# Optimization experiments

Measured on AMD Instinct MI355X. Metric: run time of the kernel, lower is better.

Reference implementation:

```python
import jax, jax.numpy as jnp
import numpy as np

N_NODES = 50000
N_GRAPHS = 500
BLOCK = N_NODES // N_GRAPHS  # 100 nodes per graph
N_EDGES = 800000
D = 32        # emb_dim = in_feat = out_feat
H = 4         # num_heads
R = 16        # num relations
N_CODES = 20000
L = 2         # n_layers
SLOPE = 0.2
LAM = 0.5     # loop_lambda


def setup_inputs() -> dict:
    key = jax.random.key(0)
    ks = jax.random.split(key, 20)
    node_ids = jax.random.randint(ks[0], (N_NODES,), 0, N_CODES)
    src = jax.random.randint(ks[1], (N_EDGES,), 0, N_NODES)
    # dst must live in the same graph as src (contiguous blocks of BLOCK nodes)
    off = jax.random.randint(ks[2], (N_EDGES,), 0, BLOCK)
    dst = (src // BLOCK) * BLOCK + off
    rel_type = jax.random.randint(ks[3], (N_EDGES,), 0, R)
    node2graph = jnp.repeat(jnp.arange(N_GRAPHS), BLOCK)
    state = jax.random.normal(ks[4], (N_GRAPHS, D), dtype=jnp.float32)
    readout_weight = jax.random.uniform(ks[5], (N_NODES,), dtype=jnp.float32)
    s = 1.0 / np.sqrt(D)
    code_emb = jax.random.uniform(ks[6], (N_CODES, D), minval=-1.0, maxval=1.0)
    rel_table = jax.random.uniform(ks[7], (R, D), minval=-1.0, maxval=1.0)
    W = jax.random.normal(ks[8], (L, R, D, D)) * s       # per-relation weights
    h_bias = jnp.zeros((L, D))
    Wr = jax.random.normal(ks[9], (L, D, H * D)) * s     # fc_rel_att
    br = jnp.zeros((L, H * D))
    We = jax.random.normal(ks[10], (L, D, H * D)) * s    # fc_edge_att
    be = jnp.zeros((L, H * D))
    attn_h = jax.random.normal(ks[11], (L, H, D)) * s
    attn_t = jax.random.normal(ks[12], (L, H, D)) * s
    attn_s = jax.random.normal(ks[13], (L, H, D)) * s
    attn_r = jax.random.normal(ks[14], (L, H, D)) * s
    attn_rs = jax.random.normal(ks[15], (L, H, D)) * s
    return dict(state=state, readout_weight=readout_weight, code_emb=code_emb,
                rel_table=rel_table, W=W, h_bias=h_bias, Wr=Wr, br=br, We=We, be=be,
                attn_h=attn_h, attn_t=attn_t, attn_s=attn_s, attn_r=attn_r, attn_rs=attn_rs,
                node_ids=node_ids, src=src, dst=dst, rel_type=rel_type, node2graph=node2graph)


def _forward(state, readout_weight, code_emb, rel_table, W, h_bias, Wr, br, We, be,
             attn_h, attn_t, attn_s, attn_r, attn_rs, node_ids, src, dst, rel_type, node2graph):
    lrelu = lambda x: jax.nn.leaky_relu(x, SLOPE)
    h = code_emb[node_ids]                      # [N, D]
    N = h.shape[0]
    G = state.shape[0]
    g_src = node2graph[src]                     # [E]
    rel_att = edge_att = None
    for l in range(L):
        # ---- relation attention (cal_rel_att, state path) ----
        rp = (rel_table @ Wr[l] + br[l]).reshape(R, H, D)
        sp = (state @ Wr[l] + br[l]).reshape(G, H, D)
        er = (rp * attn_r[l]).sum(-1)                       # [R, H]
        es = (sp * attn_rs[l]).sum(-1)                      # [G, H]
        ra = jax.nn.softmax(lrelu(er[None, :, :] + es[:, None, :]), axis=1)  # [G, R, H]
        rel_att = ra[g_src, rel_type]                       # [E, H]
        # ---- edge attention (cal_edge_att, state path) ----
        hp = (h @ We[l] + be[l]).reshape(N, H, D)           # multi-head src feat
        eh = (hp * attn_h[l]).sum(-1)                       # [N, H]
        et = (hp * attn_t[l]).sum(-1)                       # [N, H]
        nsp = (state[node2graph] @ We[l] + be[l]).reshape(N, H, D)
        esn = (nsp * attn_s[l]).sum(-1)                     # [N, H]
        e = lrelu(esn[src] + eh[src] + et[dst])             # [E, H]
        emax = jax.ops.segment_max(e, dst, num_segments=N)
        ex = jnp.exp(e - emax[dst])
        den = jax.ops.segment_sum(ex, dst, num_segments=N)
        edge_att = ex / den[dst]                            # edge_softmax over dst
        # ---- per-relation message: matmul(h_src, W[etype]) ----
        # transform all nodes per relation, then gather (same math as per-edge bmm)
        hW = jnp.einsum('nhd,rde->rnhe', hp, W[l])          # [R, N, H, D]
        msg = hW[rel_type, src]                             # [E, H, D]
        msg = (msg * edge_att[..., None] * rel_att[..., None]).sum(axis=1)  # [E, D]
        agg = jax.ops.segment_sum(msg, dst, num_segments=N) + h_bias[l]
        h = jax.nn.relu((1.0 - LAM) * agg + LAM * h)        # self-loop blend + relu
    x = jax.ops.segment_sum(h * readout_weight[:, None], node2graph, num_segments=G)
    return x, rel_att, edge_att


def reference(state, readout_weight, code_emb, rel_table, W, h_bias, Wr, br, We, be,
              attn_h, attn_t, attn_s, attn_r, attn_rs, node_ids, src, dst, rel_type, node2graph):
    return _forward(state, readout_weight, code_emb, rel_table, W, h_bias, Wr, br, We, be,
                    attn_h, attn_t, attn_s, attn_r, attn_rs, node_ids, src, dst, rel_type, node2graph)
```

## Files before the change

kernel.cpp:

```cpp
#include <hip/hip_runtime.h>
#include <hip/hip_fp16.h>

#define DI __device__ __forceinline__

constexpr int NGRAPH = 500;
constexpr int EDGES  = 800000;
constexpr int NNODE  = 50000;
constexpr int CAP    = 56;

constexpr size_t WI_CURS  = 0;
constexpr size_t WI_SMETA = 50048;
constexpr size_t WF_PREP  = WI_SMETA + (size_t)NNODE * CAP;
constexpr size_t WF_WFRAG = WF_PREP + 672;

constexpr int S_H    = 0;
constexpr int S_HP   = 8000;
constexpr int S_U    = 33600;
constexpr int S_EH   = 136800;
constexpr int S_ET   = 138400;
constexpr int S_DEN  = 140000;
constexpr int S_RA   = 141600;
constexpr int S_ESG  = 141856;
constexpr int S_AH   = 141872;
constexpr int S_AT   = 142384;
constexpr int S_MLDS = 142896;
constexpr int S_RP   = 151088;
constexpr int S_TOTAL = 151496;
constexpr int UROW = 516;

typedef _Float16 f16x8 __attribute__((ext_vector_type(8)));
typedef float f32x4 __attribute__((ext_vector_type(4)));

DI float lrelu(float x) { return x >= 0.f ? x : 0.2f * x; }
DI f16x8 u4_to_f16x8(uint4 u) { f16x8 r; __builtin_memcpy(&r, &u, 16); return r; }
DI f16x8 two_u2(uint2 a, uint2 b) { return u4_to_f16x8(make_uint4(a.x, a.y, b.x, b.y)); }
DI float h2f(unsigned short u) { __half hv; __builtin_memcpy(&hv, &u, 2); return __half2float(hv); }

DI int hpIdx(int n, int c) { return n * 128 + (c ^ ((n & 7) << 3)); }

__global__ void k_scatter(const int* __restrict__ src, const int* __restrict__ dst,
                          const int* __restrict__ rt, int* __restrict__ curs,
                          int* __restrict__ smeta) {
    int e = blockIdx.x * 256 + threadIdx.x;
    if (e >= EDGES) return;
    int s = src[e], d = dst[e], r = rt[e];
    int g = (unsigned)d / 100u;
    int pos = atomicAdd(&curs[d], 1);
    if (pos < CAP)
        smeta[(size_t)d * CAP + pos] = (s - g * 100) | (r << 7) | (e << 11);
}

__global__ void k_setup(const float* __restrict__ rel_table, const float* __restrict__ Wr,
                        const float* __restrict__ br, const float* __restrict__ We,
                        const float* __restrict__ be, const float* __restrict__ attn_r,
                        const float* __restrict__ attn_rs, const float* __restrict__ attn_s,
                        const float* __restrict__ W, float* __restrict__ prep,
                        uint4* __restrict__ wf) {
    __shared__ float wra[2][32][4];
    __shared__ float sbias[2][3][4];
    int b = blockIdx.x, t = threadIdx.x;
    if (b == 0) {
        {
            int l = t >> 7, k = (t >> 2) & 31, h = t & 3;
            float a = 0.f, bb = 0.f, c = 0.f;
            for (int d2 = 0; d2 < 32; ++d2) {
                float w1 = Wr[(size_t)(l*32 + k)*128 + h*32 + d2];
                float w2 = We[(size_t)(l*32 + k)*128 + h*32 + d2];
                a  += w1 * attn_r [l*128 + h*32 + d2];
                bb += w1 * attn_rs[l*128 + h*32 + d2];
                c  += w2 * attn_s [l*128 + h*32 + d2];
            }
            wra[l][k][h] = a;
            prep[128 + (l*32 + k)*4 + h] = bb;
            prep[384 + (l*32 + k)*4 + h] = c;
        }
        if (t < 24) {
            int l = t / 12, which = (t % 12) / 4, h = t % 4;
            const float* bp = (which == 2) ? be : br;
            const float* ap = (which == 0) ? attn_r : (which == 1 ? attn_rs : attn_s);
            float s = 0.f;
            for (int d2 = 0; d2 < 32; ++d2) s += bp[l*128 + h*32 + d2] * ap[l*128 + h*32 + d2];
            sbias[l][which][h] = s;
        }
        __syncthreads();
        if (t < 128) {
            int l = t >> 6, r = (t >> 2) & 15, h = t & 3;
            float s = sbias[l][0][h];
            for (int k = 0; k < 32; ++k) s += rel_table[r*32 + k] * wra[l][k][h];
            prep[(l*16 + r)*4 + h] = s;
        }
        if (t < 8) {
            int l = t >> 2, h = t & 3;
            prep[640 + l*4 + h] = sbias[l][1][h];
            prep[648 + l*4 + h] = sbias[l][2][h];
        }
    } else if (b <= 16) {
        int fi = (b - 1) * 256 + t;
        int ln = fi & 63, Nt = (fi >> 6) & 1, rel = (fi >> 7) & 15, l = fi >> 11;
        int j = Nt*16 + (ln & 15), k0 = (ln >> 4) << 3;
        unsigned short fr[8];
        #pragma unroll
        for (int i = 0; i < 8; ++i) {
            __half hv = __float2half(W[(((size_t)l*16 + rel)*32 + k0 + i)*32 + j]);
            __builtin_memcpy(&fr[i], &hv, 2);
        }
        uint4 o;
        o.x = fr[0] | ((unsigned)fr[1] << 16);
        o.y = fr[2] | ((unsigned)fr[3] << 16);
        o.z = fr[4] | ((unsigned)fr[5] << 16);
        o.w = fr[6] | ((unsigned)fr[7] << 16);
        wf[fi] = o;
    } else {
        int fi = (b - 17) * 256 + t;
        int ln = fi & 63, Nt = (fi >> 6) & 7, l = fi >> 9;
        int c = Nt*16 + (ln & 15);
        int phys = (c & 3)*32 + (c >> 2);
        int k0 = (ln >> 4) << 3;
        unsigned short fr[8];
        #pragma unroll
        for (int i = 0; i < 8; ++i) {
            __half hv = __float2half(We[(size_t)l*4096 + (k0 + i)*128 + phys]);
            __builtin_memcpy(&fr[i], &hv, 2);
        }
        uint4 o;
        o.x = fr[0] | ((unsigned)fr[1] << 16);
        o.y = fr[2] | ((unsigned)fr[3] << 16);
        o.z = fr[4] | ((unsigned)fr[5] << 16);
        o.w = fr[6] | ((unsigned)fr[7] << 16);
        wf[4096 + fi] = o;
    }
}

__global__ void __launch_bounds__(1024, 1)
k_fused(const float* __restrict__ state, const float* __restrict__ rw,
        const float* __restrict__ code_emb, const float* __restrict__ h_bias,
        const float* __restrict__ be, const float* __restrict__ attn_h,
        const float* __restrict__ attn_t, const int* __restrict__ node_ids,
        const int* __restrict__ curs, const int* __restrict__ smeta,
        const float* __restrict__ prep, const uint4* __restrict__ wf,
        float* __restrict__ xout, float* __restrict__ relOut, float* __restrict__ edgeOut) {
    extern __shared__ char smem[];
    __half* hH  = (__half*)(smem + S_H);
    __half* hpH = (__half*)(smem + S_HP);
    __half* Uh  = (__half*)(smem + S_U);
    float* ehp  = (float*)(smem + S_EH);
    float* etp  = (float*)(smem + S_ET);
    float* denp = (float*)(smem + S_DEN);
    float* rap  = (float*)(smem + S_RA);
    float* esgp = (float*)(smem + S_ESG);
    float* sAH  = (float*)(smem + S_AH);
    float* sAT  = (float*)(smem + S_AT);
    int*   mlds = (int*)(smem + S_MLDS);
    int*   rp   = (int*)(smem + S_RP);
    const uint4* wfe = wf + 4096;

    const int g = blockIdx.x;
    const int t = threadIdx.x;
    const int lane = t & 63, w = t >> 6;
    const int ln15 = lane & 15, q = lane >> 4, q8 = q << 3;
    const int MtA = w % 7, NtA = w / 7;
    const bool hasT = (w < 14);
    const int cg = w >> 1;
    const int colc = cg * 16 + ln15;
    const int physc = (colc & 3) * 32 + (colc >> 2);
    const int Mt0 = (w & 1) ? 4 : 0;
    const int Mt1 = (w & 1) ? 7 : 4;

    for (int i = t; i < 1600; i += 1024) {
        int n = i >> 4, dp = i & 15;
        int id = node_ids[g * 100 + n];
        float2 v = *(const float2*)&code_emb[(size_t)id * 32 + dp * 2];
        *(__half2*)&hH[n * 40 + dp * 2] = __floats2half2_rn(v.x, v.y);
    }
    if (t < 100) { int c = curs[g * 100 + t]; rp[t + 1] = c < CAP ? c : CAP; }
    if (t == 0) rp[0] = 0;
    __syncthreads();
    for (int o = 1; o < 128; o <<= 1) {
        int v = 0;
        if (t <= 100 && t >= o) v = rp[t - o];
        __syncthreads();
        if (t <= 100 && t >= o) rp[t] += v;
        __syncthreads();
    }
    for (int i = t; i < 100 * CAP; i += 1024) {
        int bin = i / CAP, pos = i % CAP;
        int lo = rp[bin], cnt = rp[bin + 1] - lo;
        if (pos < cnt)
            mlds[lo + pos] = smeta[(size_t)(g * 100 + bin) * CAP + pos];
    }

    for (int l = 0; l < 2; ++l) {
        __syncthreads();

        for (int i = t; i < 6450; i += 1024) ((uint4*)(smem + S_U))[i] = make_uint4(0, 0, 0, 0);
        if (t < 128) {
            sAH[t] = attn_h[l * 128 + (t & 3) * 32 + (t >> 2)];
            sAT[t] = attn_t[l * 128 + (t & 3) * 32 + (t >> 2)];
        }
        {
            uint4 bwe = wfe[(l * 8 + cg) * 64 + lane];
            f16x8 bw = u4_to_f16x8(bwe);
            float beC = be[l * 128 + physc];
            f32x4 z = {0.f, 0.f, 0.f, 0.f};
            for (int Mt = Mt0; Mt < Mt1; ++Mt) {
                const __half* hr = hH + (Mt * 16 + ln15) * 40 + q8;
                f32x4 pc = __builtin_amdgcn_mfma_f32_16x16x32_f16(
                    two_u2(*(const uint2*)hr, *(const uint2*)(hr + 4)), bw, z, 0, 0, 0);
                #pragma unroll
                for (int i = 0; i < 4; ++i) {
                    int n = Mt * 16 + q * 4 + i;
                    if (n < 100) hpH[hpIdx(n, colc)] = __float2half(pc[i] + beC);
                }
            }
        }
        {
            int k32 = lane & 31;
            float sG = state[g * 32 + k32];
            float4 frs = *(const float4*)&prep[128 + l * 128 + k32 * 4];
            float4 fes = *(const float4*)&prep[384 + l * 128 + k32 * 4];
            float p0 = sG * frs.x, p1 = sG * frs.y, p2 = sG * frs.z, p3 = sG * frs.w;
            float q0 = sG * fes.x, q1 = sG * fes.y, q2 = sG * fes.z, q3 = sG * fes.w;
            #pragma unroll
            for (int m = 1; m < 32; m <<= 1) {
                p0 += __shfl_xor(p0, m); p1 += __shfl_xor(p1, m);
                p2 += __shfl_xor(p2, m); p3 += __shfl_xor(p3, m);
                q0 += __shfl_xor(q0, m); q1 += __shfl_xor(q1, m);
                q2 += __shfl_xor(q2, m); q3 += __shfl_xor(q3, m);
            }
            int h = lane & 3;
            float esh  = (h & 2) ? ((h & 1) ? p3 : p2) : ((h & 1) ? p1 : p0);
            float esgh = (h & 2) ? ((h & 1) ? q3 : q2) : ((h & 1) ? q1 : q0);
            esh  += prep[640 + l * 4 + h];
            esgh += prep[648 + l * 4 + h];
            if (lane < 4) esgp[lane] = esgh;
            float er = prep[l * 64 + lane];
            float ex = __expf(lrelu(er + esh));
            float s = ex;
            s += __shfl_xor(s, 4); s += __shfl_xor(s, 8);
            s += __shfl_xor(s, 16); s += __shfl_xor(s, 32);
            rap[lane] = ex / s;
        }
        __syncthreads();

        if (t < 100) {
            int s = t;
            int sw = (s & 7) << 3;
            float eh[4] = {0, 0, 0, 0}, et[4] = {0, 0, 0, 0};
            #pragma unroll 4
            for (int i = 0; i < 16; ++i) {
                uint4 hv = *(const uint4*)&hpH[s * 128 + ((i * 8) ^ sw)];
                unsigned short hu[8];
                __builtin_memcpy(hu, &hv, 16);
                #pragma unroll
                for (int k = 0; k < 8; ++k) {
                    float f = h2f(hu[k]);
                    eh[k & 3] += f * sAH[i * 8 + k];
                    et[k & 3] += f * sAT[i * 8 + k];
                }
            }
            *(float4*)&ehp[s * 4] = make_float4(eh[0], eh[1], eh[2], eh[3]);
            *(float4*)&etp[s * 4] = make_float4(et[0], et[1], et[2], et[3]);
        }
        __syncthreads();

        if (t < 400) {
            int d = t >> 2, h = t & 3;
            int lo = rp[d], hi = rp[d + 1];
            float etd = etp[d * 4 + h] + esgp[h];
            float den = 0.f;
            for (int e = lo; e < hi; ++e) {
                int m = mlds[e];
                den += __expf(lrelu(ehp[(m & 127) * 4 + h] + etd));
            }
            denp[d * 4 + h] = den;
            if (l == 1) {
                float inv = 1.f / den;
                for (int e = lo; e < hi; ++e) {
                    int m = mlds[e];
                    float x = __expf(lrelu(ehp[(m & 127) * 4 + h] + etd));
                    int oe = (m >> 11) & 0xFFFFF;
                    int r = (m >> 7) & 15;
                    edgeOut[(size_t)oe * 4 + h] = x * inv;
                    relOut[(size_t)oe * 4 + h] = rap[r * 4 + h];
                }
            }
        }
        __syncthreads();

        if (t < 800) {
            int d = t >> 3, j = t & 7;
            int lo = rp[d], hi = rp[d + 1];
            float4 et4 = *(const float4*)&etp[d * 4];
            float4 esg4 = *(const float4*)esgp;
            float e0 = et4.x + esg4.x, e1 = et4.y + esg4.y;
            float e2 = et4.z + esg4.z, e3 = et4.w + esg4.w;
            float4 dn = *(const float4*)&denp[d * 4];
            float i0 = 1.f / dn.x, i1 = 1.f / dn.y, i2 = 1.f / dn.z, i3 = 1.f / dn.w;
            for (int e = lo; e < hi; ++e) {
                int m = mlds[e];
                int s = m & 127, r = (m >> 7) & 15;
                float4 eh4 = *(const float4*)&ehp[s * 4];
                float4 r4 = *(const float4*)&rap[r * 4];
                float c0 = __expf(lrelu(eh4.x + e0)) * i0 * r4.x;
                float c1 = __expf(lrelu(eh4.y + e1)) * i1 * r4.y;
                float c2 = __expf(lrelu(eh4.z + e2)) * i2 * r4.z;
                float c3 = __expf(lrelu(eh4.w + e3)) * i3 * r4.w;
                int sw = (s & 7) << 3;
                uint4 hv0 = *(const uint4*)&hpH[s * 128 + ((j * 16) ^ sw)];
                uint4 hv1 = *(const uint4*)&hpH[s * 128 + ((j * 16 + 8) ^ sw)];
                unsigned short hu[16];
                __builtin_memcpy(hu, &hv0, 16);
                __builtin_memcpy(hu + 8, &hv1, 16);
                float v0 = c0*h2f(hu[0])  + c1*h2f(hu[1])  + c2*h2f(hu[2])  + c3*h2f(hu[3]);
                float v1 = c0*h2f(hu[4])  + c1*h2f(hu[5])  + c2*h2f(hu[6])  + c3*h2f(hu[7]);
                float v2 = c0*h2f(hu[8])  + c1*h2f(hu[9])  + c2*h2f(hu[10]) + c3*h2f(hu[11]);
                float v3 = c0*h2f(hu[12]) + c1*h2f(hu[13]) + c2*h2f(hu[14]) + c3*h2f(hu[15]);
                __half* up = Uh + d * UROW + r * 32 + j * 4;
                __half2 u01 = *(__half2*)up;
                __half2 u23 = *(__half2*)(up + 2);
                float2 f01 = __half22float2(u01), f23 = __half22float2(u23);
                *(__half2*)up       = __floats2half2_rn(f01.x + v0, f01.y + v1);
                *(__half2*)(up + 2) = __floats2half2_rn(f23.x + v2, f23.y + v3);
            }
        }
        __syncthreads();

        f32x4 accA = {0.f, 0.f, 0.f, 0.f};
        if (hasT) {
            #pragma unroll 4
            for (int rel = 0; rel < 16; ++rel) {
                uint4 bAu = wf[((l * 16 + rel) * 2 + NtA) * 64 + lane];
                const __half* up = Uh + (MtA * 16 + ln15) * UROW + rel * 32 + q8;
                f16x8 af = two_u2(*(const uint2*)up, *(const uint2*)(up + 4));
                accA = __builtin_amdgcn_mfma_f32_16x16x32_f16(af, u4_to_f16x8(bAu), accA, 0, 0, 0);
            }
        }
        if (hasT) {
            int dcol = NtA * 16 + ln15;
            float bias = h_bias[l * 32 + dcol];
            #pragma unroll
            for (int i = 0; i < 4; ++i) {
                int n = MtA * 16 + q * 4 + i;
                if (n < 100) {
                    float hold = __half2float(hH[n * 40 + dcol]);
                    float hn = fmaxf(0.f, 0.5f * (accA[i] + bias) + 0.5f * hold);
                    hH[n * 40 + dcol] = __float2half(hn);
                }
            }
        }
    }
    __syncthreads();

    float* redp = (float*)(smem + S_U);
    {
        int part = t >> 5, d = t & 31;
        float acc = 0.f;
        for (int n = part; n < 100; n += 32)
            acc += __half2float(hH[n * 40 + d]) * rw[g * 100 + n];
        redp[part * 32 + d] = acc;
    }
    __syncthreads();
    if (t < 32) {
        float s = 0.f;
        #pragma unroll
        for (int p = 0; p < 32; ++p) s += redp[p * 32 + t];
        xout[g * 32 + t] = s;
    }
}

extern "C" void kernel_launch(void* const* d_in, const int* in_sizes, int n_in,
                              void* d_out, int out_size, void* d_ws, size_t ws_size,
                              hipStream_t stream) {
    const float* state     = (const float*)d_in[0];
    const float* rw        = (const float*)d_in[1];
    const float* code_emb  = (const float*)d_in[2];
    const float* rel_table = (const float*)d_in[3];
    const float* W         = (const float*)d_in[4];
    const float* h_bias    = (const float*)d_in[5];
    const float* Wr        = (const float*)d_in[6];
    const float* br        = (const float*)d_in[7];
    const float* We        = (const float*)d_in[8];
    const float* be        = (const float*)d_in[9];
    const float* attn_h    = (const float*)d_in[10];
    const float* attn_t    = (const float*)d_in[11];
    const float* attn_s    = (const float*)d_in[12];
    const float* attn_r    = (const float*)d_in[13];
    const float* attn_rs   = (const float*)d_in[14];
    const int* node_ids    = (const int*)d_in[15];
    const int* src         = (const int*)d_in[16];
    const int* dst         = (const int*)d_in[17];
    const int* rtype       = (const int*)d_in[18];

    float* out = (float*)d_out;
    float* xout = out;
    float* relOut = out + (size_t)NGRAPH * 32;
    float* edgeOut = relOut + (size_t)EDGES * 4;

    int* wsi = (int*)d_ws;
    float* wsf = (float*)d_ws;
    int* curs   = wsi + WI_CURS;
    int* smeta  = wsi + WI_SMETA;
    float* prep = wsf + WF_PREP;
    uint4* wfrag = (uint4*)(wsf + WF_WFRAG);

    (void)hipMemsetAsync(curs, 0, NNODE * sizeof(int), stream);
    k_scatter<<<(EDGES + 255) / 256, 256, 0, stream>>>(src, dst, rtype, curs, smeta);
    k_setup<<<21, 256, 0, stream>>>(rel_table, Wr, br, We, be, attn_r, attn_rs, attn_s,
                                    W, prep, wfrag);

    (void)hipFuncSetAttribute((const void*)k_fused, hipFuncAttributeMaxDynamicSharedMemorySize, S_TOTAL);
    k_fused<<<NGRAPH, 1024, S_TOTAL, stream>>>(state, rw, code_emb, h_bias, be,
                                               attn_h, attn_t, node_ids, curs, smeta,
                                               prep, wfrag, xout, relOut, edgeOut);
}
```

Measured before the change: 195.8 us.

## Merge scatter and setup kernels, fuse attention output writes, use fdot2 aggregation

Merges the edge-scatter and weight-setup kernels into a single launch, using block index ranges to pick the role. The layer-1 edge_att and rel_att output writes move out of the denominator loop and into the message loop, done by one lane per destination as float4 stores, so the exponentials are no longer computed twice. The per-edge message accumulation now packs the four head coefficients to fp16 and uses fdot2 with half2 adds instead of per-element half-to-float conversions. Rounding the coefficients to fp16 before the dot product adds some precision loss.

```diff
diff --git a/kernel.cpp b/kernel.cpp
--- a/kernel.cpp
+++ b/kernel.cpp
@@ -7,6 +7,7 @@
 constexpr int EDGES  = 800000;
 constexpr int NNODE  = 50000;
 constexpr int CAP    = 56;
+constexpr int SCAT_BLOCKS = (EDGES + 255) / 256;
 
 constexpr size_t WI_CURS  = 0;
 constexpr size_t WI_SMETA = 50048;
@@ -29,6 +30,7 @@
 constexpr int UROW = 516;
 
 typedef _Float16 f16x8 __attribute__((ext_vector_type(8)));
+typedef _Float16 f16x2 __attribute__((ext_vector_type(2)));
 typedef float f32x4 __attribute__((ext_vector_type(4)));
 
 DI float lrelu(float x) { return x >= 0.f ? x : 0.2f * x; }
@@ -36,42 +38,51 @@
 DI f16x8 two_u2(uint2 a, uint2 b) { return u4_to_f16x8(make_uint4(a.x, a.y, b.x, b.y)); }
 DI float h2f(unsigned short u) { __half hv; __builtin_memcpy(&hv, &u, 2); return __half2float(hv); }
 
+DI float fdot2u(unsigned a, unsigned b, float c) {
+    f16x2 av, bv;
+    __builtin_memcpy(&av, &a, 4);
+    __builtin_memcpy(&bv, &b, 4);
+    return __builtin_amdgcn_fdot2(av, bv, c, false);
+}
+
 DI int hpIdx(int n, int c) { return n * 128 + (c ^ ((n & 7) << 3)); }
 
-__global__ void k_scatter(const int* __restrict__ src, const int* __restrict__ dst,
-                          const int* __restrict__ rt, int* __restrict__ curs,
-                          int* __restrict__ smeta) {
-    int e = blockIdx.x * 256 + threadIdx.x;
-    if (e >= EDGES) return;
-    int s = src[e], d = dst[e], r = rt[e];
-    int g = (unsigned)d / 100u;
-    int pos = atomicAdd(&curs[d], 1);
-    if (pos < CAP)
-        smeta[(size_t)d * CAP + pos] = (s - g * 100) | (r << 7) | (e << 11);
-}
-
-__global__ void k_setup(const float* __restrict__ rel_table, const float* __restrict__ Wr,
-                        const float* __restrict__ br, const float* __restrict__ We,
-                        const float* __restrict__ be, const float* __restrict__ attn_r,
-                        const float* __restrict__ attn_rs, const float* __restrict__ attn_s,
-                        const float* __restrict__ W, float* __restrict__ prep,
-                        uint4* __restrict__ wf) {
+__global__ void k_prep(const int* __restrict__ src, const int* __restrict__ dst,
+                       const int* __restrict__ rt, int* __restrict__ curs,
+                       int* __restrict__ smeta,
+                       const float* __restrict__ rel_table, const float* __restrict__ Wr,
+                       const float* __restrict__ br, const float* __restrict__ We,
+                       const float* __restrict__ be, const float* __restrict__ attn_r,
+                       const float* __restrict__ attn_rs, const float* __restrict__ attn_s,
+                       const float* __restrict__ W, float* __restrict__ prep,
+                       uint4* __restrict__ wf) {
     __shared__ float wra[2][32][4];
     __shared__ float sbias[2][3][4];
-    int b = blockIdx.x, t = threadIdx.x;
+    int bb = blockIdx.x, t = threadIdx.x;
+    if (bb < SCAT_BLOCKS) {
+        int e = bb * 256 + t;
+        if (e >= EDGES) return;
+        int s = src[e], d = dst[e], r = rt[e];
+        int g = (unsigned)d / 100u;
+        int pos = atomicAdd(&curs[d], 1);
+        if (pos < CAP)
+            smeta[(size_t)d * CAP + pos] = (s - g * 100) | (r << 7) | (e << 11);
+        return;
+    }
+    int b = bb - SCAT_BLOCKS;
     if (b == 0) {
         {
             int l = t >> 7, k = (t >> 2) & 31, h = t & 3;
-            float a = 0.f, bb = 0.f, c = 0.f;
+            float a = 0.f, b2 = 0.f, c = 0.f;
             for (int d2 = 0; d2 < 32; ++d2) {
                 float w1 = Wr[(size_t)(l*32 + k)*128 + h*32 + d2];
                 float w2 = We[(size_t)(l*32 + k)*128 + h*32 + d2];
                 a  += w1 * attn_r [l*128 + h*32 + d2];
-                bb += w1 * attn_rs[l*128 + h*32 + d2];
+                b2 += w1 * attn_rs[l*128 + h*32 + d2];
                 c  += w2 * attn_s [l*128 + h*32 + d2];
             }
             wra[l][k][h] = a;
-            prep[128 + (l*32 + k)*4 + h] = bb;
+            prep[128 + (l*32 + k)*4 + h] = b2;
             prep[384 + (l*32 + k)*4 + h] = c;
         }
         if (t < 24) {
@@ -273,17 +284,6 @@
                 den += __expf(lrelu(ehp[(m & 127) * 4 + h] + etd));
             }
             denp[d * 4 + h] = den;
-            if (l == 1) {
-                float inv = 1.f / den;
-                for (int e = lo; e < hi; ++e) {
-                    int m = mlds[e];
-                    float x = __expf(lrelu(ehp[(m & 127) * 4 + h] + etd));
-                    int oe = (m >> 11) & 0xFFFFF;
-                    int r = (m >> 7) & 15;
-                    edgeOut[(size_t)oe * 4 + h] = x * inv;
-                    relOut[(size_t)oe * 4 + h] = rap[r * 4 + h];
-                }
-            }
         }
         __syncthreads();
 
@@ -296,31 +296,38 @@
             float e2 = et4.z + esg4.z, e3 = et4.w + esg4.w;
             float4 dn = *(const float4*)&denp[d * 4];
             float i0 = 1.f / dn.x, i1 = 1.f / dn.y, i2 = 1.f / dn.z, i3 = 1.f / dn.w;
+            bool wAtt = (l == 1) && (j == 0);
             for (int e = lo; e < hi; ++e) {
                 int m = mlds[e];
                 int s = m & 127, r = (m >> 7) & 15;
                 float4 eh4 = *(const float4*)&ehp[s * 4];
                 float4 r4 = *(const float4*)&rap[r * 4];
-                float c0 = __expf(lrelu(eh4.x + e0)) * i0 * r4.x;
-                float c1 = __expf(lrelu(eh4.y + e1)) * i1 * r4.y;
-                float c2 = __expf(lrelu(eh4.z + e2)) * i2 * r4.z;
-                float c3 = __expf(lrelu(eh4.w + e3)) * i3 * r4.w;
+                float a0 = __expf(lrelu(eh4.x + e0)) * i0;
+                float a1 = __expf(lrelu(eh4.y + e1)) * i1;
+                float a2 = __expf(lrelu(eh4.z + e2)) * i2;
+                float a3 = __expf(lrelu(eh4.w + e3)) * i3;
+                if (wAtt) {
+                    int oe = (m >> 11) & 0xFFFFF;
+                    *(float4*)&edgeOut[(size_t)oe * 4] = make_float4(a0, a1, a2, a3);
+                    *(float4*)&relOut[(size_t)oe * 4] = r4;
+                }
+                __half2 c01h = __floats2half2_rn(a0 * r4.x, a1 * r4.y);
+                __half2 c23h = __floats2half2_rn(a2 * r4.z, a3 * r4.w);
+                unsigned uc01, uc23;
+                __builtin_memcpy(&uc01, &c01h, 4);
+                __builtin_memcpy(&uc23, &c23h, 4);
                 int sw = (s & 7) << 3;
                 uint4 hv0 = *(const uint4*)&hpH[s * 128 + ((j * 16) ^ sw)];
                 uint4 hv1 = *(const uint4*)&hpH[s * 128 + ((j * 16 + 8) ^ sw)];
-                unsigned short hu[16];
-                __builtin_memcpy(hu, &hv0, 16);
-                __builtin_memcpy(hu + 8, &hv1, 16);
-                float v0 = c0*h2f(hu[0])  + c1*h2f(hu[1])  + c2*h2f(hu[2])  + c3*h2f(hu[3]);
-                float v1 = c0*h2f(hu[4])  + c1*h2f(hu[5])  + c2*h2f(hu[6])  + c3*h2f(hu[7]);
-                float v2 = c0*h2f(hu[8])  + c1*h2f(hu[9])  + c2*h2f(hu[10]) + c3*h2f(hu[11]);
-                float v3 = c0*h2f(hu[12]) + c1*h2f(hu[13]) + c2*h2f(hu[14]) + c3*h2f(hu[15]);
-                __half* up = Uh + d * UROW + r * 32 + j * 4;
-                __half2 u01 = *(__half2*)up;
-                __half2 u23 = *(__half2*)(up + 2);
-                float2 f01 = __half22float2(u01), f23 = __half22float2(u23);
-                *(__half2*)up       = __floats2half2_rn(f01.x + v0, f01.y + v1);
-                *(__half2*)(up + 2) = __floats2half2_rn(f23.x + v2, f23.y + v3);
+                float v0 = fdot2u(uc01, hv0.x, fdot2u(uc23, hv0.y, 0.f));
+                float v1 = fdot2u(uc01, hv0.z, fdot2u(uc23, hv0.w, 0.f));
+                float v2 = fdot2u(uc01, hv1.x, fdot2u(uc23, hv1.y, 0.f));
+                float v3 = fdot2u(uc01, hv1.z, fdot2u(uc23, hv1.w, 0.f));
+                __half2 v01 = __floats2half2_rn(v0, v1);
+                __half2 v23 = __floats2half2_rn(v2, v3);
+                __half2* up = (__half2*)(Uh + d * UROW + r * 32 + j * 4);
+                up[0] = __hadd2(up[0], v01);
+                up[1] = __hadd2(up[1], v23);
             }
         }
         __syncthreads();
@@ -404,9 +411,9 @@
     uint4* wfrag = (uint4*)(wsf + WF_WFRAG);
 
     (void)hipMemsetAsync(curs, 0, NNODE * sizeof(int), stream);
-    k_scatter<<<(EDGES + 255) / 256, 256, 0, stream>>>(src, dst, rtype, curs, smeta);
-    k_setup<<<21, 256, 0, stream>>>(rel_table, Wr, br, We, be, attn_r, attn_rs, attn_s,
-                                    W, prep, wfrag);
+    k_prep<<<SCAT_BLOCKS + 21, 256, 0, stream>>>(src, dst, rtype, curs, smeta,
+                                                 rel_table, Wr, br, We, be,
+                                                 attn_r, attn_rs, attn_s, W, prep, wfrag);
 
     (void)hipFuncSetAttribute((const void*)k_fused, hipFuncAttributeMaxDynamicSharedMemorySize, S_TOTAL);
     k_fused<<<NGRAPH, 1024, S_TOTAL, stream>>>(state, rw, code_emb, h_bias, be,
```

After: 173.3 us. -11.5%, faster.
